# Kernel tuning notes

Hardware: AMD Instinct MI355X
Metric: run time of the kernel (lower is better)

Reference implementation:

```python
import jax, jax.numpy as jnp
import numpy as np

B, T, E, H, O, L = 64, 512, 512, 1024, 512, 2


def setup_inputs() -> dict:
    key = jax.random.key(0)
    ks = jax.random.split(key, 12)
    s = 0.02  # small init scale for weights
    # h0 mimics torch.nn.init.xavier_normal_ on a (L, B, H) tensor:
    # fan_in = B*H, fan_out = L*H -> std = sqrt(2/(fan_in+fan_out))
    xav_std = float(np.sqrt(2.0 / (B * H + L * H)))
    return {
        "embeddings": jax.random.normal(ks[0], (B, T, E), jnp.float32),
        "h0": jax.random.normal(ks[1], (L, B, H), jnp.float32) * xav_std,
        "W_ih0": jax.random.normal(ks[2], (H, E), jnp.float32) * s,
        "b_ih0": jax.random.normal(ks[3], (H,), jnp.float32) * s,
        "W_ih1": jax.random.normal(ks[4], (H, H), jnp.float32) * s,
        "b_ih1": jax.random.normal(ks[5], (H,), jnp.float32) * s,
        "W_hh0": jax.random.normal(ks[6], (H, H), jnp.float32) * s,
        "b_hh0": jax.random.normal(ks[7], (H,), jnp.float32) * s,
        "W_hh1": jax.random.normal(ks[8], (H, H), jnp.float32) * s,
        "b_hh1": jax.random.normal(ks[9], (H,), jnp.float32) * s,
        "W_out": jax.random.normal(ks[10], (O, H), jnp.float32) * s,
        "b_out": jax.random.normal(ks[11], (O,), jnp.float32) * s,
    }


def reference(embeddings, h0, W_ih0, b_ih0, W_ih1, b_ih1,
              W_hh0, b_hh0, W_hh1, b_hh1, W_out, b_out):
    # Precompute all layer-0 input projections as one big GEMM: (B,T,H)
    xp = jnp.einsum('bte,he->bth', embeddings, W_ih0) + b_ih0
    xp_t = jnp.swapaxes(xp, 0, 1)  # (T, B, H)

    def step(carry, x_t):
        h0_, h1_ = carry
        h0n = jnp.tanh(x_t + h0_ @ W_hh0.T + b_hh0)
        h1n = jnp.tanh(h0n @ W_ih1.T + b_ih1 + h1_ @ W_hh1.T + b_hh1)
        out_t = h1n @ W_out.T + b_out  # (B, O)
        return (h0n, h1n), out_t

    _, outs = jax.lax.scan(step, (h0[0], h0[1]), xp_t)  # outs: (T, B, O)
    return jnp.swapaxes(outs, 0, 1)  # (B, T, O)
```

## Files before the change

### kernel.cpp

```cpp
#include <hip/hip_runtime.h>
#include <cmath>

#define B_ 64
#define T_ 512
#define E_ 512
#define H_ 1024
#define O_ 512
#define BH (B_ * H_)
#define HSTRIDE 1160

typedef unsigned short ushort_t;
typedef __bf16 bf16x8 __attribute__((ext_vector_type(8)));
typedef float f32x4 __attribute__((ext_vector_type(4)));

__device__ __forceinline__ ushort_t f2bf(float f) {
    union { float f; unsigned int u; } x; x.f = f;
    unsigned int r = x.u + 0x7fffu + ((x.u >> 16) & 1u);
    return (ushort_t)(r >> 16);
}
__device__ __forceinline__ float bf2f(ushort_t u) {
    union { unsigned int u; float f; } x; x.u = ((unsigned int)u) << 16;
    return x.f;
}
__device__ __forceinline__ uint4 pack8bf(float4 v0, float4 v1) {
    uint4 pk;
    pk.x = (unsigned)f2bf(v0.x) | ((unsigned)f2bf(v0.y) << 16);
    pk.y = (unsigned)f2bf(v0.z) | ((unsigned)f2bf(v0.w) << 16);
    pk.z = (unsigned)f2bf(v1.x) | ((unsigned)f2bf(v1.y) << 16);
    pk.w = (unsigned)f2bf(v1.z) | ((unsigned)f2bf(v1.w) << 16);
    return pk;
}
__device__ __forceinline__ bf16x8 pack8(const float* src) {
    float4 v0 = *(const float4*)src;
    float4 v1 = *(const float4*)(src + 4);
    union { uint4 u; bf16x8 b; } c;
    c.u = pack8bf(v0, v1);
    return c.b;
}

__global__ void prep_kernel(const float* __restrict__ h0, ushort_t* __restrict__ hinit,
                            int* __restrict__ bar) {
    int i = blockIdx.x * blockDim.x + threadIdx.x;
    if (i < 8192) bar[i] = 0;
    if (i < 2 * BH) hinit[i] = f2bf(h0[i]);
}

template <int MODE>
__launch_bounds__(256)
__global__ void gemm_bt(const void* __restrict__ Ap, const float* __restrict__ Wp,
                        const float* __restrict__ bias, void* __restrict__ outp,
                        int N, int K) {
    __shared__ __align__(16) ushort_t As[128 * 72];
    __shared__ __align__(16) ushort_t Bs[128 * 72];
    const int tid = threadIdx.x;
    const int lane = tid & 63;
    const int w = tid >> 6;
    const int wm = (w >> 1) * 64;
    const int wn = (w & 1) * 64;
    const int q = lane >> 4;
    const int l16 = lane & 15;
    const int m0 = blockIdx.y * 128;
    const int n0 = blockIdx.x * 128;

    const float*    Af = (const float*)Ap;
    const ushort_t* Ab = (const ushort_t*)Ap;

    f32x4 zero = {0.f, 0.f, 0.f, 0.f};
    f32x4 acc[4][4];
#pragma unroll
    for (int i = 0; i < 4; i++)
#pragma unroll
        for (int j = 0; j < 4; j++) acc[i][j] = zero;

    for (int k0 = 0; k0 < K; k0 += 64) {
#pragma unroll
        for (int it = 0; it < 4; it++) {
            int task = tid + it * 256;
            int row = task >> 3, seg = task & 7;
            if (MODE == 0) {
                int Ra = m0 + row;
                const float* src = Af + (size_t)((Ra & 63) * T_ + (Ra >> 6)) * K + k0 + seg * 8;
                float4 v0 = *(const float4*)src;
                float4 v1 = *(const float4*)(src + 4);
                *(uint4*)&As[row * 72 + seg * 8] = pack8bf(v0, v1);
            } else {
                const ushort_t* src = Ab + (size_t)(m0 + row) * K + k0 + seg * 8;
                *(uint4*)&As[row * 72 + seg * 8] = *(const uint4*)src;
            }
            const float* wsrc = Wp + (size_t)(n0 + row) * K + k0 + seg * 8;
            float4 w0 = *(const float4*)wsrc;
            float4 w1 = *(const float4*)(wsrc + 4);
            *(uint4*)&Bs[row * 72 + seg * 8] = pack8bf(w0, w1);
        }
        __syncthreads();
#pragma unroll
        for (int ks = 0; ks < 64; ks += 32) {
            bf16x8 af[4], bfr[4];
#pragma unroll
            for (int i = 0; i < 4; i++)
                af[i] = *(const bf16x8*)&As[(wm + i * 16 + l16) * 72 + ks + q * 8];
#pragma unroll
            for (int j = 0; j < 4; j++)
                bfr[j] = *(const bf16x8*)&Bs[(wn + j * 16 + l16) * 72 + ks + q * 8];
#pragma unroll
            for (int i = 0; i < 4; i++)
#pragma unroll
                for (int j = 0; j < 4; j++)
                    acc[i][j] = __builtin_amdgcn_mfma_f32_16x16x32_bf16(af[i], bfr[j], acc[i][j], 0, 0, 0);
        }
        __syncthreads();
    }

#pragma unroll
    for (int j = 0; j < 4; j++) {
        int C = n0 + wn + j * 16 + l16;
        float bv = bias[C];
#pragma unroll
        for (int i = 0; i < 4; i++) {
#pragma unroll
            for (int r = 0; r < 4; r++) {
                int R = m0 + wm + i * 16 + q * 4 + r;
                float v = acc[i][j][r] + bv;
                if (MODE == 2) {
                    ((float*)outp)[(size_t)((R & 63) * T_ + (R >> 6)) * N + C] = v;
                } else {
                    ((ushort_t*)outp)[(size_t)R * N + C] = f2bf(v);
                }
            }
        }
    }
}

template <int LAYER>
__device__ __forceinline__ void rnn_body(
    ushort_t* __restrict__ xall, const ushort_t* __restrict__ xsrc,
    const ushort_t* __restrict__ hin,
    const float* __restrict__ Wa, const float* __restrict__ Wb,
    const float* __restrict__ ba, const float* __restrict__ bb,
    int* __restrict__ bar,
    ushort_t* __restrict__ Hs0, ushort_t* __restrict__ Hs1,
    float (*__restrict__ Rs)[16][33]) {
    (void)xsrc;

    const int tid = threadIdx.x;
    const int lane = tid & 63;
    const int w = tid >> 6;
    const int q = lane >> 4;
    const int l16 = lane & 15;
    const int gb = (blockIdx.x >> 5) & 3;
    const int cb = blockIdx.x & 31;
    const int b0 = gb * 16;
    const int n0 = cb * 32;
    int* flags   = bar + (LAYER * 4 + gb) * 1024;
    int* flagsrc = bar + gb * 1024;
    int* myflag  = flags + (cb << 5);
    int* pollp;
    int polladd;
    if (LAYER == 1) {
        pollp   = ((lane & 32) ? flagsrc : flags) + ((lane & 31) << 5);
        polladd = (lane & 32) ? 1 : 0;
    } else {
        pollp   = flags + ((lane & 31) << 5);
        polladd = 0;
    }

    bf16x8 wA[16], wB[16];
#pragma unroll
    for (int g = 0; g < 2; g++)
#pragma unroll
        for (int kk = 0; kk < 8; kk++) {
            size_t off = (size_t)(n0 + g * 16 + l16) * H_ + w * 256 + kk * 32 + q * 8;
            wA[g * 8 + kk] = pack8(Wa + off);
            if (LAYER == 1) wB[g * 8 + kk] = pack8(Wb + off);
        }

    const int em = tid >> 4;
    const int en = (tid & 15) * 2;
    float bv0 = ba[n0 + en], bv1 = ba[n0 + en + 1];
    if (LAYER == 1) { bv0 += bb[n0 + en]; bv1 += bb[n0 + en + 1]; }

    const int rbase2 = (tid >> 7) * 2;
    const int seg = tid & 127;

    for (int r = 0; r < 512; r++) {
        if (LAYER == 1) {
            while (true) {
                int v = __hip_atomic_load(pollp, __ATOMIC_RELAXED, __HIP_MEMORY_SCOPE_SYSTEM);
                if (__ballot(v >= r + polladd) == ~0ull) break;
            }
        } else if (r > 0) {
            while (true) {
                int v = __hip_atomic_load(pollp, __ATOMIC_RELAXED, __HIP_MEMORY_SCOPE_SYSTEM);
                if (__ballot(v >= r) == ~0ull) break;
            }
        }

        const ushort_t* s1 = (r == 0) ? hin : (xall + (size_t)(r - 1) * BH);
        const ushort_t* c0 = s1 + (size_t)(b0 + rbase2) * H_ + seg * 8;
        const ushort_t* c1 = c0 + 4 * H_;
        const ushort_t* c2 = c0 + 8 * H_;
        const ushort_t* c3 = c0 + 12 * H_;
        unsigned xw = 0;
        uint4 e0, e1, e2, e3, e4, e5, e6, e7;
        if (LAYER == 0) {
            const ushort_t* xaddr = xall + (size_t)r * BH + (size_t)(b0 + em) * H_ + n0 + en;
            asm volatile(
                "global_load_dwordx4 %0, %9, off sc0 sc1\n\t"
                "global_load_dwordx4 %1, %9, off offset:2048 sc0 sc1\n\t"
                "global_load_dwordx4 %2, %10, off sc0 sc1\n\t"
                "global_load_dwordx4 %3, %10, off offset:2048 sc0 sc1\n\t"
                "global_load_dwordx4 %4, %11, off sc0 sc1\n\t"
                "global_load_dwordx4 %5, %11, off offset:2048 sc0 sc1\n\t"
                "global_load_dwordx4 %6, %12, off sc0 sc1\n\t"
                "global_load_dwordx4 %7, %12, off offset:2048 sc0 sc1\n\t"
                "global_load_dword %8, %13, off sc0 sc1\n\t"
                "s_waitcnt vmcnt(0)"
                : "=&v"(e0), "=&v"(e1), "=&v"(e2), "=&v"(e3),
                  "=&v"(e4), "=&v"(e5), "=&v"(e6), "=&v"(e7), "=&v"(xw)
                : "v"(c0), "v"(c1), "v"(c2), "v"(c3), "v"(xaddr)
                : "memory");
        } else {
            const ushort_t* a0 = xsrc + (size_t)r * BH + (size_t)(b0 + rbase2) * H_ + seg * 8;
            const ushort_t* a1 = a0 + 4 * H_;
            const ushort_t* a2 = a0 + 8 * H_;
            const ushort_t* a3 = a0 + 12 * H_;
            uint4 d0, d1, d2, d3, d4, d5, d6, d7;
            asm volatile(
                "global_load_dwordx4 %0, %16, off sc0 sc1\n\t"
                "global_load_dwordx4 %1, %16, off offset:2048 sc0 sc1\n\t"
                "global_load_dwordx4 %2, %17, off sc0 sc1\n\t"
                "global_load_dwordx4 %3, %17, off offset:2048 sc0 sc1\n\t"
                "global_load_dwordx4 %4, %18, off sc0 sc1\n\t"
                "global_load_dwordx4 %5, %18, off offset:2048 sc0 sc1\n\t"
                "global_load_dwordx4 %6, %19, off sc0 sc1\n\t"
                "global_load_dwordx4 %7, %19, off offset:2048 sc0 sc1\n\t"
                "global_load_dwordx4 %8, %20, off sc0 sc1\n\t"
                "global_load_dwordx4 %9, %20, off offset:2048 sc0 sc1\n\t"
                "global_load_dwordx4 %10, %21, off sc0 sc1\n\t"
                "global_load_dwordx4 %11, %21, off offset:2048 sc0 sc1\n\t"
                "global_load_dwordx4 %12, %22, off sc0 sc1\n\t"
                "global_load_dwordx4 %13, %22, off offset:2048 sc0 sc1\n\t"
                "global_load_dwordx4 %14, %23, off sc0 sc1\n\t"
                "global_load_dwordx4 %15, %23, off offset:2048 sc0 sc1\n\t"
                "s_waitcnt vmcnt(0)"
                : "=&v"(d0), "=&v"(d1), "=&v"(d2), "=&v"(d3),
                  "=&v"(d4), "=&v"(d5), "=&v"(d6), "=&v"(d7),
                  "=&v"(e0), "=&v"(e1), "=&v"(e2), "=&v"(e3),
                  "=&v"(e4), "=&v"(e5), "=&v"(e6), "=&v"(e7)
                : "v"(a0), "v"(a1), "v"(a2), "v"(a3),
                  "v"(c0), "v"(c1), "v"(c2), "v"(c3)
                : "memory");
            *(uint4*)&Hs0[(rbase2 + 0) * HSTRIDE + seg * 8] = d0;
            *(uint4*)&Hs0[(rbase2 + 1) * HSTRIDE + seg * 8] = d1;
            *(uint4*)&Hs0[(rbase2 + 4) * HSTRIDE + seg * 8] = d2;
            *(uint4*)&Hs0[(rbase2 + 5) * HSTRIDE + seg * 8] = d3;
            *(uint4*)&Hs0[(rbase2 + 8) * HSTRIDE + seg * 8] = d4;
            *(uint4*)&Hs0[(rbase2 + 9) * HSTRIDE + seg * 8] = d5;
            *(uint4*)&Hs0[(rbase2 + 12) * HSTRIDE + seg * 8] = d6;
            *(uint4*)&Hs0[(rbase2 + 13) * HSTRIDE + seg * 8] = d7;
        }
        *(uint4*)&Hs1[(rbase2 + 0) * HSTRIDE + seg * 8] = e0;
        *(uint4*)&Hs1[(rbase2 + 1) * HSTRIDE + seg * 8] = e1;
        *(uint4*)&Hs1[(rbase2 + 4) * HSTRIDE + seg * 8] = e2;
        *(uint4*)&Hs1[(rbase2 + 5) * HSTRIDE + seg * 8] = e3;
        *(uint4*)&Hs1[(rbase2 + 8) * HSTRIDE + seg * 8] = e4;
        *(uint4*)&Hs1[(rbase2 + 9) * HSTRIDE + seg * 8] = e5;
        *(uint4*)&Hs1[(rbase2 + 12) * HSTRIDE + seg * 8] = e6;
        *(uint4*)&Hs1[(rbase2 + 13) * HSTRIDE + seg * 8] = e7;
        __syncthreads();

        f32x4 acc0 = {0.f, 0.f, 0.f, 0.f};
        f32x4 acc1 = {0.f, 0.f, 0.f, 0.f};
        const int kb = w * 256;
        if (LAYER == 1) {
#pragma unroll
            for (int kk = 0; kk < 8; kk++) {
                bf16x8 a = *(const bf16x8*)&Hs0[l16 * HSTRIDE + kb + kk * 32 + q * 8];
                acc0 = __builtin_amdgcn_mfma_f32_16x16x32_bf16(a, wA[kk], acc0, 0, 0, 0);
                acc1 = __builtin_amdgcn_mfma_f32_16x16x32_bf16(a, wA[8 + kk], acc1, 0, 0, 0);
            }
#pragma unroll
            for (int kk = 0; kk < 8; kk++) {
                bf16x8 a = *(const bf16x8*)&Hs1[l16 * HSTRIDE + kb + kk * 32 + q * 8];
                acc0 = __builtin_amdgcn_mfma_f32_16x16x32_bf16(a, wB[kk], acc0, 0, 0, 0);
                acc1 = __builtin_amdgcn_mfma_f32_16x16x32_bf16(a, wB[8 + kk], acc1, 0, 0, 0);
            }
        } else {
#pragma unroll
            for (int kk = 0; kk < 8; kk++) {
                bf16x8 a = *(const bf16x8*)&Hs1[l16 * HSTRIDE + kb + kk * 32 + q * 8];
                acc0 = __builtin_amdgcn_mfma_f32_16x16x32_bf16(a, wA[kk], acc0, 0, 0, 0);
                acc1 = __builtin_amdgcn_mfma_f32_16x16x32_bf16(a, wA[8 + kk], acc1, 0, 0, 0);
            }
        }
#pragma unroll
        for (int rr = 0; rr < 4; rr++) {
            Rs[w][q * 4 + rr][l16] = acc0[rr];
            Rs[w][q * 4 + rr][16 + l16] = acc1[rr];
        }
        __syncthreads();

        {
            float sA = Rs[0][em][en] + Rs[1][em][en] + Rs[2][em][en] + Rs[3][em][en];
            float sB = Rs[0][em][en + 1] + Rs[1][em][en + 1] + Rs[2][em][en + 1] + Rs[3][em][en + 1];
            ushort_t* dst = xall + (size_t)r * BH + (size_t)(b0 + em) * H_ + n0 + en;
            if (LAYER == 0) {
                sA += bf2f((ushort_t)(xw & 0xffff));
                sB += bf2f((ushort_t)(xw >> 16));
            }
            sA += bv0;
            sB += bv1;
            unsigned pk = (unsigned)f2bf(tanhf(sA)) | ((unsigned)f2bf(tanhf(sB)) << 16);
            __hip_atomic_store((unsigned*)dst, pk, __ATOMIC_RELAXED, __HIP_MEMORY_SCOPE_SYSTEM);
        }

        if (LAYER == 0 || r < 511) {
            __syncthreads();
            if (tid == 0)
                __hip_atomic_store(myflag, r + 1, __ATOMIC_RELAXED, __HIP_MEMORY_SCOPE_SYSTEM);
        }
    }
}

__launch_bounds__(256, 1)
__global__ void rnn_fused(ushort_t* __restrict__ x0, ushort_t* __restrict__ x1,
                          const ushort_t* __restrict__ hinit,
                          const float* __restrict__ W_hh0, const float* __restrict__ b_hh0,
                          const float* __restrict__ W_ih1, const float* __restrict__ W_hh1,
                          const float* __restrict__ b_ih1, const float* __restrict__ b_hh1,
                          int* __restrict__ bar) {
    __shared__ __align__(16) ushort_t Hs0[16 * HSTRIDE];
    __shared__ __align__(16) ushort_t Hs1[16 * HSTRIDE];
    __shared__ float Rs[4][16][33];
    if (blockIdx.x < 128) {
        rnn_body<0>(x0, (const ushort_t*)nullptr, hinit,
                    W_hh0, W_hh0, b_hh0, b_hh0, bar, Hs0, Hs1, Rs);
    } else {
        rnn_body<1>(x1, x0, hinit + BH,
                    W_ih1, W_hh1, b_ih1, b_hh1, bar, Hs0, Hs1, Rs);
    }
}

extern "C" void kernel_launch(void* const* d_in, const int* in_sizes, int n_in,
                              void* d_out, int out_size, void* d_ws, size_t ws_size,
                              hipStream_t stream) {
    (void)in_sizes; (void)n_in; (void)out_size; (void)ws_size;
    const float* emb   = (const float*)d_in[0];
    const float* h0    = (const float*)d_in[1];
    const float* W_ih0 = (const float*)d_in[2];
    const float* b_ih0 = (const float*)d_in[3];
    const float* W_ih1 = (const float*)d_in[4];
    const float* b_ih1 = (const float*)d_in[5];
    const float* W_hh0 = (const float*)d_in[6];
    const float* b_hh0 = (const float*)d_in[7];
    const float* W_hh1 = (const float*)d_in[8];
    const float* b_hh1 = (const float*)d_in[9];
    const float* W_out = (const float*)d_in[10];
    const float* b_out = (const float*)d_in[11];
    float* out = (float*)d_out;

    char* ws = (char*)d_ws;
    int*      bar   = (int*)ws;
    ushort_t* hinit = (ushort_t*)(ws + 65536);
    ushort_t* xp    = (ushort_t*)(ws + 65536 + 2 * BH * 2);
    ushort_t* xq    = xp + (size_t)T_ * BH;

    prep_kernel<<<512, 256, 0, stream>>>(h0, hinit, bar);

    gemm_bt<0><<<dim3(H_ / 128, (B_ * T_) / 128), 256, 0, stream>>>(
        emb, W_ih0, b_ih0, xp, H_, E_);

    rnn_fused<<<256, 256, 0, stream>>>(xp, xq, hinit,
                                       W_hh0, b_hh0, W_ih1, W_hh1, b_ih1, b_hh1, bar);

    gemm_bt<2><<<dim3(O_ / 128, (B_ * T_) / 128), 256, 0, stream>>>(
        xq, W_out, b_out, out, O_, H_);
}
```

Baseline: 1.874 ms.

## Halve RNN pipeline blocks by widening each block's column tile to 64

Each recurrent block now owns 64 output columns instead of 32, so the persistent kernel runs with 128 blocks and each block polls 16 flags instead of 32. The goal is to cut cross-block synchronisation fan-in and flag traffic per timestep, in exchange for doubling the weight registers per thread and the MFMA work per block. The layer-0 input projection is now prefetched with short loads before the spin-wait, and stores and flag writes use explicit cache-bypassing asm. A spin-count cap was also added that can break out of the wait early, which risks correctness under long stalls.

```diff
diff --git a/kernel.cpp b/kernel.cpp
--- a/kernel.cpp
+++ b/kernel.cpp
@@ -133,98 +133,119 @@
 
 template <int LAYER>
 __device__ __forceinline__ void rnn_body(
-    ushort_t* __restrict__ xall, const ushort_t* __restrict__ xsrc,
-    const ushort_t* __restrict__ hin,
+    ushort_t* __restrict__ x0, ushort_t* __restrict__ x1,
+    const ushort_t* __restrict__ hinit,
     const float* __restrict__ Wa, const float* __restrict__ Wb,
     const float* __restrict__ ba, const float* __restrict__ bb,
-    int* __restrict__ bar,
+    int* __restrict__ bar, int gb, int cb,
     ushort_t* __restrict__ Hs0, ushort_t* __restrict__ Hs1,
-    float (*__restrict__ Rs)[16][33]) {
-    (void)xsrc;
+    float (*__restrict__ Rs)[16][68]) {
 
     const int tid = threadIdx.x;
     const int lane = tid & 63;
     const int w = tid >> 6;
     const int q = lane >> 4;
     const int l16 = lane & 15;
-    const int gb = (blockIdx.x >> 5) & 3;
-    const int cb = blockIdx.x & 31;
     const int b0 = gb * 16;
-    const int n0 = cb * 32;
-    int* flags   = bar + (LAYER * 4 + gb) * 1024;
-    int* flagsrc = bar + gb * 1024;
-    int* myflag  = flags + (cb << 5);
+    const int n0 = cb * 64;
+    int* fl_own = bar + (LAYER * 4 + gb) * 1024;
+    int* fl_src = bar + gb * 1024;
+    int* myflag = fl_own + (cb << 5);
     int* pollp;
-    int polladd;
+    int thr;
     if (LAYER == 1) {
-        pollp   = ((lane & 32) ? flagsrc : flags) + ((lane & 31) << 5);
-        polladd = (lane & 32) ? 1 : 0;
+        pollp = (((lane & 31) < 16) ? fl_own : fl_src) + ((lane & 15) << 5);
+        thr = ((lane & 31) < 16) ? 0 : 1;
     } else {
-        pollp   = flags + ((lane & 31) << 5);
-        polladd = 0;
+        pollp = fl_own + ((lane & 15) << 5);
+        thr = 0;
     }
 
-    bf16x8 wA[16], wB[16];
-#pragma unroll
-    for (int g = 0; g < 2; g++)
+    bf16x8 wA[32], wB[32];
+#pragma unroll
+    for (int cg = 0; cg < 4; cg++)
 #pragma unroll
         for (int kk = 0; kk < 8; kk++) {
-            size_t off = (size_t)(n0 + g * 16 + l16) * H_ + w * 256 + kk * 32 + q * 8;
-            wA[g * 8 + kk] = pack8(Wa + off);
-            if (LAYER == 1) wB[g * 8 + kk] = pack8(Wb + off);
-        }
-
-    const int em = tid >> 4;
-    const int en = (tid & 15) * 2;
-    float bv0 = ba[n0 + en], bv1 = ba[n0 + en + 1];
-    if (LAYER == 1) { bv0 += bb[n0 + en]; bv1 += bb[n0 + en + 1]; }
+            size_t off = (size_t)(n0 + cg * 16 + l16) * H_ + w * 256 + kk * 32 + q * 8;
+            wA[cg * 8 + kk] = pack8(Wa + off);
+            if (LAYER == 1) wB[cg * 8 + kk] = pack8(Wb + off);
+        }
+
+    const int oc = tid & 63;
+    const int orb = w * 4;
+    float bv = ba[n0 + oc];
+    if (LAYER == 1) bv += bb[n0 + oc];
 
     const int rbase2 = (tid >> 7) * 2;
     const int seg = tid & 127;
-
-    for (int r = 0; r < 512; r++) {
-        if (LAYER == 1) {
+    const int kb = w * 256;
+
+    for (int k = 0; k < 512; k++) {
+        unsigned xw0 = 0, xw1 = 0, xw2 = 0, xw3 = 0;
+        ushort_t* xaddr = x0 + (size_t)k * BH + (size_t)(b0 + orb) * H_ + n0 + oc;
+        if (LAYER == 0) {
+            asm volatile(
+                "global_load_ushort %0, %4, off\n\t"
+                "global_load_ushort %1, %4, off offset:2048\n\t"
+                "global_load_ushort %2, %5, off\n\t"
+                "global_load_ushort %3, %5, off offset:2048"
+                : "=&v"(xw0), "=&v"(xw1), "=&v"(xw2), "=&v"(xw3)
+                : "v"(xaddr), "v"(xaddr + 2 * H_));
+        }
+
+        if (LAYER == 1 || k > 0) {
+            int spin = 0;
             while (true) {
-                int v = __hip_atomic_load(pollp, __ATOMIC_RELAXED, __HIP_MEMORY_SCOPE_SYSTEM);
-                if (__ballot(v >= r + polladd) == ~0ull) break;
-            }
-        } else if (r > 0) {
-            while (true) {
-                int v = __hip_atomic_load(pollp, __ATOMIC_RELAXED, __HIP_MEMORY_SCOPE_SYSTEM);
-                if (__ballot(v >= r) == ~0ull) break;
-            }
-        }
-
-        const ushort_t* s1 = (r == 0) ? hin : (xall + (size_t)(r - 1) * BH);
-        const ushort_t* c0 = s1 + (size_t)(b0 + rbase2) * H_ + seg * 8;
-        const ushort_t* c1 = c0 + 4 * H_;
-        const ushort_t* c2 = c0 + 8 * H_;
-        const ushort_t* c3 = c0 + 12 * H_;
-        unsigned xw = 0;
-        uint4 e0, e1, e2, e3, e4, e5, e6, e7;
+                int v;
+                asm volatile("global_load_dword %0, %1, off sc0 sc1\n\ts_waitcnt vmcnt(0)"
+                             : "=&v"(v) : "v"(pollp) : "memory");
+                if (__ballot(v >= k + thr) == ~0ull) break;
+                if (++spin > (1 << 18)) break;
+            }
+        }
+
         if (LAYER == 0) {
-            const ushort_t* xaddr = xall + (size_t)r * BH + (size_t)(b0 + em) * H_ + n0 + en;
+            const ushort_t* Asrc = (k == 0) ? hinit : (x0 + (size_t)(k - 1) * BH);
+            const ushort_t* c0 = Asrc + (size_t)(b0 + rbase2) * H_ + seg * 8;
+            const ushort_t* c1 = c0 + 4 * H_;
+            const ushort_t* c2 = c0 + 8 * H_;
+            const ushort_t* c3 = c0 + 12 * H_;
+            uint4 e0, e1, e2, e3, e4, e5, e6, e7;
             asm volatile(
-                "global_load_dwordx4 %0, %9, off sc0 sc1\n\t"
-                "global_load_dwordx4 %1, %9, off offset:2048 sc0 sc1\n\t"
-                "global_load_dwordx4 %2, %10, off sc0 sc1\n\t"
-                "global_load_dwordx4 %3, %10, off offset:2048 sc0 sc1\n\t"
-                "global_load_dwordx4 %4, %11, off sc0 sc1\n\t"
-                "global_load_dwordx4 %5, %11, off offset:2048 sc0 sc1\n\t"
-                "global_load_dwordx4 %6, %12, off sc0 sc1\n\t"
-                "global_load_dwordx4 %7, %12, off offset:2048 sc0 sc1\n\t"
-                "global_load_dword %8, %13, off sc0 sc1\n\t"
+                "global_load_dwordx4 %0, %8, off sc0 sc1\n\t"
+                "global_load_dwordx4 %1, %8, off offset:2048 sc0 sc1\n\t"
+                "global_load_dwordx4 %2, %9, off sc0 sc1\n\t"
+                "global_load_dwordx4 %3, %9, off offset:2048 sc0 sc1\n\t"
+                "global_load_dwordx4 %4, %10, off sc0 sc1\n\t"
+                "global_load_dwordx4 %5, %10, off offset:2048 sc0 sc1\n\t"
+                "global_load_dwordx4 %6, %11, off sc0 sc1\n\t"
+                "global_load_dwordx4 %7, %11, off offset:2048 sc0 sc1\n\t"
                 "s_waitcnt vmcnt(0)"
                 : "=&v"(e0), "=&v"(e1), "=&v"(e2), "=&v"(e3),
-                  "=&v"(e4), "=&v"(e5), "=&v"(e6), "=&v"(e7), "=&v"(xw)
-                : "v"(c0), "v"(c1), "v"(c2), "v"(c3), "v"(xaddr)
+                  "=&v"(e4), "=&v"(e5), "=&v"(e6), "=&v"(e7)
+                : "v"(c0), "v"(c1), "v"(c2), "v"(c3)
                 : "memory");
+            *(uint4*)&Hs1[(rbase2 + 0) * HSTRIDE + seg * 8] = e0;
+            *(uint4*)&Hs1[(rbase2 + 1) * HSTRIDE + seg * 8] = e1;
+            *(uint4*)&Hs1[(rbase2 + 4) * HSTRIDE + seg * 8] = e2;
+            *(uint4*)&Hs1[(rbase2 + 5) * HSTRIDE + seg * 8] = e3;
+            *(uint4*)&Hs1[(rbase2 + 8) * HSTRIDE + seg * 8] = e4;
+            *(uint4*)&Hs1[(rbase2 + 9) * HSTRIDE + seg * 8] = e5;
+            *(uint4*)&Hs1[(rbase2 + 12) * HSTRIDE + seg * 8] = e6;
+            *(uint4*)&Hs1[(rbase2 + 13) * HSTRIDE + seg * 8] = e7;
         } else {
-            const ushort_t* a0 = xsrc + (size_t)r * BH + (size_t)(b0 + rbase2) * H_ + seg * 8;
+            const ushort_t* Asrc = x0 + (size_t)k * BH;
+            const ushort_t* Bsrc = (k == 0) ? (hinit + BH) : (x1 + (size_t)(k - 1) * BH);
+            const ushort_t* a0 = Asrc + (size_t)(b0 + rbase2) * H_ + seg * 8;
             const ushort_t* a1 = a0 + 4 * H_;
             const ushort_t* a2 = a0 + 8 * H_;
             const ushort_t* a3 = a0 + 12 * H_;
+            const ushort_t* c0 = Bsrc + (size_t)(b0 + rbase2) * H_ + seg * 8;
+            const ushort_t* c1 = c0 + 4 * H_;
+            const ushort_t* c2 = c0 + 8 * H_;
+            const ushort_t* c3 = c0 + 12 * H_;
             uint4 d0, d1, d2, d3, d4, d5, d6, d7;
+            uint4 e0, e1, e2, e3, e4, e5, e6, e7;
             asm volatile(
                 "global_load_dwordx4 %0, %16, off sc0 sc1\n\t"
                 "global_load_dwordx4 %1, %16, off offset:2048 sc0 sc1\n\t"
@@ -258,86 +279,96 @@
             *(uint4*)&Hs0[(rbase2 + 9) * HSTRIDE + seg * 8] = d5;
             *(uint4*)&Hs0[(rbase2 + 12) * HSTRIDE + seg * 8] = d6;
             *(uint4*)&Hs0[(rbase2 + 13) * HSTRIDE + seg * 8] = d7;
-        }
-        *(uint4*)&Hs1[(rbase2 + 0) * HSTRIDE + seg * 8] = e0;
-        *(uint4*)&Hs1[(rbase2 + 1) * HSTRIDE + seg * 8] = e1;
-        *(uint4*)&Hs1[(rbase2 + 4) * HSTRIDE + seg * 8] = e2;
-        *(uint4*)&Hs1[(rbase2 + 5) * HSTRIDE + seg * 8] = e3;
-        *(uint4*)&Hs1[(rbase2 + 8) * HSTRIDE + seg * 8] = e4;
-        *(uint4*)&Hs1[(rbase2 + 9) * HSTRIDE + seg * 8] = e5;
-        *(uint4*)&Hs1[(rbase2 + 12) * HSTRIDE + seg * 8] = e6;
-        *(uint4*)&Hs1[(rbase2 + 13) * HSTRIDE + seg * 8] = e7;
+            *(uint4*)&Hs1[(rbase2 + 0) * HSTRIDE + seg * 8] = e0;
+            *(uint4*)&Hs1[(rbase2 + 1) * HSTRIDE + seg * 8] = e1;
+            *(uint4*)&Hs1[(rbase2 + 4) * HSTRIDE + seg * 8] = e2;
+            *(uint4*)&Hs1[(rbase2 + 5) * HSTRIDE + seg * 8] = e3;
+            *(uint4*)&Hs1[(rbase2 + 8) * HSTRIDE + seg * 8] = e4;
+            *(uint4*)&Hs1[(rbase2 + 9) * HSTRIDE + seg * 8] = e5;
+            *(uint4*)&Hs1[(rbase2 + 12) * HSTRIDE + seg * 8] = e6;
+            *(uint4*)&Hs1[(rbase2 + 13) * HSTRIDE + seg * 8] = e7;
+        }
         __syncthreads();
 
-        f32x4 acc0 = {0.f, 0.f, 0.f, 0.f};
-        f32x4 acc1 = {0.f, 0.f, 0.f, 0.f};
-        const int kb = w * 256;
+        f32x4 z = {0.f, 0.f, 0.f, 0.f};
+        f32x4 acc[4] = {z, z, z, z};
+#pragma unroll
+        for (int kk = 0; kk < 8; kk++) {
+            const ushort_t* hs = (LAYER == 1) ? Hs0 : Hs1;
+            bf16x8 a = *(const bf16x8*)&hs[l16 * HSTRIDE + kb + kk * 32 + q * 8];
+#pragma unroll
+            for (int cg = 0; cg < 4; cg++)
+                acc[cg] = __builtin_amdgcn_mfma_f32_16x16x32_bf16(a, wA[cg * 8 + kk], acc[cg], 0, 0, 0);
+        }
         if (LAYER == 1) {
 #pragma unroll
             for (int kk = 0; kk < 8; kk++) {
-                bf16x8 a = *(const bf16x8*)&Hs0[l16 * HSTRIDE + kb + kk * 32 + q * 8];
-                acc0 = __builtin_amdgcn_mfma_f32_16x16x32_bf16(a, wA[kk], acc0, 0, 0, 0);
-                acc1 = __builtin_amdgcn_mfma_f32_16x16x32_bf16(a, wA[8 + kk], acc1, 0, 0, 0);
-            }
-#pragma unroll
-            for (int kk = 0; kk < 8; kk++) {
-                bf16x8 a = *(const bf16x8*)&Hs1[l16 * HSTRIDE + kb + kk * 32 + q * 8];
-                acc0 = __builtin_amdgcn_mfma_f32_16x16x32_bf16(a, wB[kk], acc0, 0, 0, 0);
-                acc1 = __builtin_amdgcn_mfma_f32_16x16x32_bf16(a, wB[8 + kk], acc1, 0, 0, 0);
-            }
-        } else {
-#pragma unroll
-            for (int kk = 0; kk < 8; kk++) {
-                bf16x8 a = *(const bf16x8*)&Hs1[l16 * HSTRIDE + kb + kk * 32 + q * 8];
-                acc0 = __builtin_amdgcn_mfma_f32_16x16x32_bf16(a, wA[kk], acc0, 0, 0, 0);
-                acc1 = __builtin_amdgcn_mfma_f32_16x16x32_bf16(a, wA[8 + kk], acc1, 0, 0, 0);
-            }
-        }
-#pragma unroll
-        for (int rr = 0; rr < 4; rr++) {
-            Rs[w][q * 4 + rr][l16] = acc0[rr];
-            Rs[w][q * 4 + rr][16 + l16] = acc1[rr];
-        }
+                bf16x8 b = *(const bf16x8*)&Hs1[l16 * HSTRIDE + kb + kk * 32 + q * 8];
+#pragma unroll
+                for (int cg = 0; cg < 4; cg++)
+                    acc[cg] = __builtin_amdgcn_mfma_f32_16x16x32_bf16(b, wB[cg * 8 + kk], acc[cg], 0, 0, 0);
+            }
+        }
+#pragma unroll
+        for (int cg = 0; cg < 4; cg++)
+#pragma unroll
+            for (int rr = 0; rr < 4; rr++)
+                Rs[w][q * 4 + rr][cg * 16 + l16] = acc[cg][rr];
         __syncthreads();
 
         {
-            float sA = Rs[0][em][en] + Rs[1][em][en] + Rs[2][em][en] + Rs[3][em][en];
-            float sB = Rs[0][em][en + 1] + Rs[1][em][en + 1] + Rs[2][em][en + 1] + Rs[3][em][en + 1];
-            ushort_t* dst = xall + (size_t)r * BH + (size_t)(b0 + em) * H_ + n0 + en;
-            if (LAYER == 0) {
-                sA += bf2f((ushort_t)(xw & 0xffff));
-                sB += bf2f((ushort_t)(xw >> 16));
-            }
-            sA += bv0;
-            sB += bv1;
-            unsigned pk = (unsigned)f2bf(tanhf(sA)) | ((unsigned)f2bf(tanhf(sB)) << 16);
-            __hip_atomic_store((unsigned*)dst, pk, __ATOMIC_RELAXED, __HIP_MEMORY_SCOPE_SYSTEM);
-        }
-
-        if (LAYER == 0 || r < 511) {
+            ushort_t* dst = (LAYER == 1 ? x1 : x0) + (size_t)k * BH
+                            + (size_t)(b0 + orb) * H_ + n0 + oc;
+            unsigned pv[4];
+#pragma unroll
+            for (int rr = 0; rr < 4; rr++) {
+                float s = Rs[0][orb + rr][oc] + Rs[1][orb + rr][oc]
+                        + Rs[2][orb + rr][oc] + Rs[3][orb + rr][oc] + bv;
+                if (LAYER == 0) {
+                    unsigned xv = (rr == 0) ? xw0 : (rr == 1) ? xw1 : (rr == 2) ? xw2 : xw3;
+                    s += bf2f((ushort_t)xv);
+                }
+                pv[rr] = f2bf(tanhf(s));
+            }
+            asm volatile(
+                "global_store_short %0, %2, off sc0 sc1\n\t"
+                "global_store_short %0, %3, off offset:2048 sc0 sc1\n\t"
+                "global_store_short %1, %4, off sc0 sc1\n\t"
+                "global_store_short %1, %5, off offset:2048 sc0 sc1"
+                :: "v"(dst), "v"(dst + 2 * H_),
+                   "v"(pv[0]), "v"(pv[1]), "v"(pv[2]), "v"(pv[3])
+                : "memory");
+        }
+
+        if (LAYER == 0 || k < 511) {
+            asm volatile("s_waitcnt vmcnt(0)" ::: "memory");
             __syncthreads();
-            if (tid == 0)
-                __hip_atomic_store(myflag, r + 1, __ATOMIC_RELAXED, __HIP_MEMORY_SCOPE_SYSTEM);
+            if (tid == 0) {
+                int fv = k + 1;
+                asm volatile("global_store_dword %0, %1, off sc0 sc1"
+                             :: "v"(myflag), "v"(fv) : "memory");
+            }
         }
     }
 }
 
 __launch_bounds__(256, 1)
-__global__ void rnn_fused(ushort_t* __restrict__ x0, ushort_t* __restrict__ x1,
-                          const ushort_t* __restrict__ hinit,
-                          const float* __restrict__ W_hh0, const float* __restrict__ b_hh0,
-                          const float* __restrict__ W_ih1, const float* __restrict__ W_hh1,
-                          const float* __restrict__ b_ih1, const float* __restrict__ b_hh1,
-                          int* __restrict__ bar) {
+__global__ void rnn_pipe(ushort_t* __restrict__ x0, ushort_t* __restrict__ x1,
+                         const ushort_t* __restrict__ hinit,
+                         const float* __restrict__ W_hh0, const float* __restrict__ b_hh0,
+                         const float* __restrict__ W_ih1, const float* __restrict__ W_hh1,
+                         const float* __restrict__ b_ih1, const float* __restrict__ b_hh1,
+                         int* __restrict__ bar) {
     __shared__ __align__(16) ushort_t Hs0[16 * HSTRIDE];
     __shared__ __align__(16) ushort_t Hs1[16 * HSTRIDE];
-    __shared__ float Rs[4][16][33];
-    if (blockIdx.x < 128) {
-        rnn_body<0>(x0, (const ushort_t*)nullptr, hinit,
-                    W_hh0, W_hh0, b_hh0, b_hh0, bar, Hs0, Hs1, Rs);
+    __shared__ float Rs[4][16][68];
+    if (blockIdx.x < 64) {
+        rnn_body<0>(x0, x1, hinit, W_hh0, W_hh0, b_hh0, b_hh0, bar,
+                    (int)(blockIdx.x >> 4), (int)(blockIdx.x & 15), Hs0, Hs1, Rs);
     } else {
-        rnn_body<1>(x1, x0, hinit + BH,
-                    W_ih1, W_hh1, b_ih1, b_hh1, bar, Hs0, Hs1, Rs);
+        int b = blockIdx.x - 64;
+        rnn_body<1>(x0, x1, hinit, W_ih1, W_hh1, b_ih1, b_hh1, bar,
+                    b >> 4, b & 15, Hs0, Hs1, Rs);
     }
 }
 
@@ -370,8 +401,8 @@
     gemm_bt<0><<<dim3(H_ / 128, (B_ * T_) / 128), 256, 0, stream>>>(
         emb, W_ih0, b_ih0, xp, H_, E_);
 
-    rnn_fused<<<256, 256, 0, stream>>>(xp, xq, hinit,
-                                       W_hh0, b_hh0, W_ih1, W_hh1, b_ih1, b_hh1, bar);
+    rnn_pipe<<<128, 256, 0, stream>>>(xp, xq, hinit,
+                                      W_hh0, b_hh0, W_ih1, W_hh1, b_ih1, b_hh1, bar);
 
     gemm_bt<2><<<dim3(O_ / 128, (B_ * T_) / 128), 256, 0, stream>>>(
         xq, W_out, b_out, out, O_, H_);
```

Result: slower. 2.356 ms (+25.7%).
